# Performance work log

Measured on AMD Instinct MI355X. Metric: run time of the kernel, lower is better.

The kernel has to match this reference:

```python
import jax, jax.numpy as jnp
from jax import lax
import numpy as np

BETA = 1.0


def setup_inputs() -> dict:
    key = jax.random.key(0)
    k1, k2, k3, k4, k5, k6 = jax.random.split(key, 6)
    B, S, D = 16, 2048, 768
    encoder_outputs = jax.random.normal(k1, (B, S, D), dtype=jnp.float32)
    encoder_lens = jax.random.randint(k2, (B,), 1, S + 1, dtype=jnp.int32)
    # AlphaNetwork params: Conv1d(D, D, kernel=3, padding same) + Linear(D, 1)
    conv_w = jax.random.normal(k3, (D, D, 3), dtype=jnp.float32) * (1.0 / np.sqrt(3 * D))
    conv_b = jax.random.normal(k4, (D,), dtype=jnp.float32) * 0.01
    lin_w = jax.random.normal(k5, (1, D), dtype=jnp.float32) * (1.0 / np.sqrt(D))
    lin_b = jax.random.normal(k6, (1,), dtype=jnp.float32) * 0.01
    return {"encoder_outputs": encoder_outputs, "encoder_lens": encoder_lens,
            "conv_w": conv_w, "conv_b": conv_b, "lin_w": lin_w, "lin_b": lin_b}


def _alpha_network(x, conv_w, conv_b, lin_w, lin_b):
    # x: (B, S, D) -> alphas (B, S)
    x_ncw = jnp.transpose(x, (0, 2, 1))  # (B, D, S)
    y = lax.conv_general_dilated(x_ncw, conv_w, window_strides=(1,), padding="SAME",
                                 dimension_numbers=("NCH", "OIH", "NCH"))
    y = y + conv_b[None, :, None]
    y = jnp.transpose(y, (0, 2, 1))  # (B, S, D)
    return jax.nn.sigmoid(jnp.einsum("bsd,od->bso", y, lin_w) + lin_b)[..., 0]


def _cif_single(h, alpha, length, beta=BETA):
    # h: (S, D), alpha: (S,), length: scalar int
    S, D = h.shape

    def step(carry, inputs):
        aacc, hacc = carry
        a_u, h_u, t = inputs
        valid = t < length
        aacc_u = aacc + a_u
        fire = (aacc_u >= beta) & valid
        a1 = 1.0 - aacc               # weight assigned to h_u for the emitted segment
        c = hacc + a1 * h_u           # emitted vector on fire
        a2 = a_u - a1                 # leftover weight carried to next segment
        new_aacc = jnp.where(fire, a2, jnp.where(valid, aacc_u, aacc))
        new_hacc = jnp.where(fire, a2 * h_u, jnp.where(valid, hacc + a_u * h_u, hacc))
        return (new_aacc, new_hacc), (fire, jnp.where(fire, c, jnp.zeros_like(c)))

    init = (jnp.zeros((), h.dtype), jnp.zeros((D,), h.dtype))
    _, (fired, cs) = lax.scan(step, init, (alpha, h, jnp.arange(S)))
    # compact fired vectors to the front; non-fired rows scatter to dropped bucket S
    pos = jnp.cumsum(fired.astype(jnp.int32)) - 1
    idx = jnp.where(fired, pos, S)
    out = jnp.zeros((S + 1, D), h.dtype).at[idx].set(cs)[:S]
    return out, jnp.sum(fired.astype(jnp.int32))


def reference(encoder_outputs, encoder_lens, conv_w, conv_b, lin_w, lin_b):
    alphas = _alpha_network(encoder_outputs, conv_w, conv_b, lin_w, lin_b)  # (B, S)
    output_c, len_tensor = jax.vmap(_cif_single)(encoder_outputs, alphas, encoder_lens)
    # output_c padded to seq_len (static upper bound on number of fires)
    return output_c, len_tensor
```

## Files before the change

### kernel.cpp

```cpp
#include <hip/hip_runtime.h>
#include <math.h>

#define BB 16
#define SS 2048
#define DD 768
#define NROW (BB * SS)
#define NSLICE 16

#define PART_OFF  0
#define W3_OFF    (PART_OFF + NSLICE*2304)
#define BIAS_OFF  (W3_OFF + 2304)
#define E0_OFF    (BIAS_OFF + 64)
#define E1_OFF    (E0_OFF + NROW)
#define E2_OFF    (E1_OFF + NROW)
#define WCUR_OFF  (E2_OFF + NROW)
#define WNEXT_OFF (WCUR_OFF + NROW)
#define FT_OFF    (WNEXT_OFF + NROW)
#define LEN_OFF   (FT_OFF + NROW)

__global__ __launch_bounds__(256) void k1a_fold_part(
    const float* __restrict__ conv_w, const float* __restrict__ lin_w,
    float* __restrict__ ws) {
  int tid = threadIdx.x;
  int slice = blockIdx.x / 9, cb = blockIdx.x % 9;
  int c = cb * 256 + tid;
  int o0 = slice * (DD / NSLICE);
  float acc = 0.f;
#pragma unroll 4
  for (int oo = 0; oo < DD / NSLICE; ++oo) {
    int o = o0 + oo;
    acc = fmaf(lin_w[o], conv_w[(size_t)o * 2304 + c], acc);
  }
  ws[PART_OFF + slice * 2304 + c] = acc;
}

__global__ __launch_bounds__(256) void k1r_fold_reduce(
    const float* __restrict__ conv_b, const float* __restrict__ lin_w,
    const float* __restrict__ lin_b, float* __restrict__ ws) {
  __shared__ float red[256];
  int tid = threadIdx.x;
  if (blockIdx.x < 9) {
    int c = blockIdx.x * 256 + tid;
    float acc = 0.f;
#pragma unroll
    for (int s = 0; s < NSLICE; ++s) acc += ws[PART_OFF + s * 2304 + c];
    int i = c / 3, k = c % 3;
    ws[W3_OFF + k * DD + i] = acc;
  } else {
    float p = 0.f;
    for (int o = tid; o < DD; o += 256) p = fmaf(lin_w[o], conv_b[o], p);
    red[tid] = p;
    __syncthreads();
    for (int off = 128; off > 0; off >>= 1) {
      if (tid < off) red[tid] += red[tid + off];
      __syncthreads();
    }
    if (tid == 0) ws[BIAS_OFF] = red[0] + lin_b[0];
  }
}

__global__ __launch_bounds__(256) void k2a_dots(
    const float* __restrict__ x, const float* __restrict__ ws,
    const int* __restrict__ lens,
    float* __restrict__ e0, float* __restrict__ e1, float* __restrict__ e2) {
  __shared__ float w3[2304];
  int tid = threadIdx.x;
  int wave = tid >> 6, lane = tid & 63;
  int row = blockIdx.x * 4 + wave;
  int b = row >> 11, s = row & (SS - 1);
  bool active = (s <= lens[b]);
  for (int c = tid; c < 2304; c += 256) w3[c] = ws[W3_OFF + c];
  __syncthreads();
  if (!active) return;
  const float4* xr = (const float4*)(x + (size_t)row * DD);
  const float4* w0p = (const float4*)(w3);
  const float4* w1p = (const float4*)(w3 + DD);
  const float4* w2p = (const float4*)(w3 + 2 * DD);
  float a0 = 0.f, a1 = 0.f, a2 = 0.f;
#pragma unroll
  for (int q = 0; q < 3; ++q) {
    int f = lane + q * 64;
    float4 xv = xr[f];
    float4 w0 = w0p[f], w1 = w1p[f], w2 = w2p[f];
    a0 += w0.x * xv.x + w0.y * xv.y + w0.z * xv.z + w0.w * xv.w;
    a1 += w1.x * xv.x + w1.y * xv.y + w1.z * xv.z + w1.w * xv.w;
    a2 += w2.x * xv.x + w2.y * xv.y + w2.z * xv.z + w2.w * xv.w;
  }
#pragma unroll
  for (int m = 1; m < 64; m <<= 1) {
    a0 += __shfl_xor(a0, m);
    a1 += __shfl_xor(a1, m);
    a2 += __shfl_xor(a2, m);
  }
  if (lane == 0) { e0[row] = a0; e1[row] = a1; e2[row] = a2; }
}

__global__ __launch_bounds__(256) void k3_scan(
    const float* __restrict__ ws_ro, const int* __restrict__ lens,
    float* __restrict__ wcur, float* __restrict__ wnext, int* __restrict__ ft,
    int* __restrict__ lenws, float* __restrict__ out_len) {
  __shared__ double wtot[4];
  int b = blockIdx.x, tid = threadIdx.x;
  int wave = tid >> 6, lane = tid & 63;
  const float* e0 = ws_ro + E0_OFF + b * SS;
  const float* e1 = ws_ro + E1_OFF + b * SS;
  const float* e2 = ws_ro + E2_OFF + b * SS;
  float bias = ws_ro[BIAS_OFF];
  int len = lens[b];
  int t0 = tid * 8;
  float a[8];
  double incl[8];
  double run = 0.0;
#pragma unroll
  for (int e = 0; e < 8; ++e) {
    int t = t0 + e;
    float av = 0.f;
    if (t < len) {
      float z = bias + e1[t];
      if (t > 0) z += e0[t - 1];
      z += e2[t + 1];
      av = 1.f / (1.f + expf(-z));
    }
    a[e] = av;
    run += (double)av;
    incl[e] = run;
  }
  double v = run;
#pragma unroll
  for (int m = 1; m < 64; m <<= 1) {
    double o = __shfl_up(v, m);
    if (lane >= m) v += o;
  }
  if (lane == 63) wtot[wave] = v;
  __syncthreads();
  double woff = 0.0;
  for (int w = 0; w < wave; ++w) woff += wtot[w];
  double excl = woff + v - run;
  double Pprev = excl;
  int Fprev = (int)floor(excl);
#pragma unroll
  for (int e = 0; e < 8; ++e) {
    int t = t0 + e;
    double P = excl + incl[e];
    int F = (int)floor(P);
    bool fire = (F > Fprev);
    float wc = fire ? (float)((double)F - Pprev) : a[e];
    float wn = fire ? (float)(P - (double)F) : 0.f;
    wcur[b * SS + t] = wc;
    wnext[b * SS + t] = wn;
    if (fire) ft[b * SS + (F - 1)] = t;
    Pprev = P;
    Fprev = F;
  }
  if (tid == 255) {
    int L = (int)floor(woff + v);
    lenws[b] = L;
    out_len[b] = (float)L;
  }
}

__global__ __launch_bounds__(256) void k4_emit(
    const float* __restrict__ x, const float* __restrict__ wcur,
    const float* __restrict__ wnext, const int* __restrict__ ft,
    const int* __restrict__ lenws, float* __restrict__ out) {
  int tid = threadIdx.x, wave = tid >> 6, lane = tid & 63;
  int row = blockIdx.x * 4 + wave;
  int b = row >> 11, j = row & (SS - 1);
  float4* orow = (float4*)(out + (size_t)row * DD);
  int L = lenws[b];
  if (j >= L) {
    float4 z = {0.f, 0.f, 0.f, 0.f};
    orow[lane] = z;
    orow[lane + 64] = z;
    orow[lane + 128] = z;
    return;
  }
  int start = (j == 0) ? 0 : ft[b * SS + j - 1];
  int end = ft[b * SS + j];
  float4 acc0 = {0, 0, 0, 0}, acc1 = {0, 0, 0, 0}, acc2 = {0, 0, 0, 0};
  for (int t = start; t <= end; ++t) {
    float w = (j > 0 && t == start) ? wnext[b * SS + t] : wcur[b * SS + t];
    const float4* xr = (const float4*)(x + ((size_t)b * SS + t) * DD);
    float4 v0 = xr[lane], v1 = xr[lane + 64], v2 = xr[lane + 128];
    acc0.x = fmaf(w, v0.x, acc0.x); acc0.y = fmaf(w, v0.y, acc0.y);
    acc0.z = fmaf(w, v0.z, acc0.z); acc0.w = fmaf(w, v0.w, acc0.w);
    acc1.x = fmaf(w, v1.x, acc1.x); acc1.y = fmaf(w, v1.y, acc1.y);
    acc1.z = fmaf(w, v1.z, acc1.z); acc1.w = fmaf(w, v1.w, acc1.w);
    acc2.x = fmaf(w, v2.x, acc2.x); acc2.y = fmaf(w, v2.y, acc2.y);
    acc2.z = fmaf(w, v2.z, acc2.z); acc2.w = fmaf(w, v2.w, acc2.w);
  }
  orow[lane] = acc0;
  orow[lane + 64] = acc1;
  orow[lane + 128] = acc2;
}

extern "C" void kernel_launch(void* const* d_in, const int* in_sizes, int n_in,
                              void* d_out, int out_size, void* d_ws, size_t ws_size,
                              hipStream_t stream) {
  const float* x      = (const float*)d_in[0];
  const int*   lens   = (const int*)d_in[1];
  const float* conv_w = (const float*)d_in[2];
  const float* conv_b = (const float*)d_in[3];
  const float* lin_w  = (const float*)d_in[4];
  const float* lin_b  = (const float*)d_in[5];
  float* out = (float*)d_out;
  float* ws = (float*)d_ws;

  float* e0 = ws + E0_OFF;
  float* e1 = ws + E1_OFF;
  float* e2 = ws + E2_OFF;
  float* wc = ws + WCUR_OFF;
  float* wn = ws + WNEXT_OFF;
  int* ft = (int*)(ws + FT_OFF);
  int* lenws = (int*)(ws + LEN_OFF);
  float* out_len = out + (size_t)NROW * DD;

  k1a_fold_part<<<NSLICE * 9, 256, 0, stream>>>(conv_w, lin_w, ws);
  k1r_fold_reduce<<<10, 256, 0, stream>>>(conv_b, lin_w, lin_b, ws);
  k2a_dots<<<NROW / 4, 256, 0, stream>>>(x, ws, lens, e0, e1, e2);
  k3_scan<<<BB, 256, 0, stream>>>(ws, lens, wc, wn, ft, lenws, out_len);
  k4_emit<<<NROW / 4, 256, 0, stream>>>(x, wc, wn, ft, lenws, out);
}
```

Measured before the change: 202.4 us.

## Fuse dot and scan kernels via last-block atomic counter, pack weights, nontemporal stores

Merges the per-row dot-product kernel and the per-batch scan kernel into one launch. Each block bumps a per-batch atomic counter, and the last block to arrive for a batch runs the scan, which removes a kernel launch and its serialization gap. The current and next weights are packed into one float2 array so the emit loop does a single load. The emit kernel now writes its outputs with nontemporal stores and uses native vector FMAs. The cost is that 16 blocks run a serial scan at the tail of a large grid, which could lengthen the critical path.

```diff
diff --git a/kernel.cpp b/kernel.cpp
--- a/kernel.cpp
+++ b/kernel.cpp
@@ -7,21 +7,24 @@
 #define NROW (BB * SS)
 #define NSLICE 16
 
+typedef float nfloat4 __attribute__((ext_vector_type(4)));
+
 #define PART_OFF  0
 #define W3_OFF    (PART_OFF + NSLICE*2304)
 #define BIAS_OFF  (W3_OFF + 2304)
-#define E0_OFF    (BIAS_OFF + 64)
+#define CNT_OFF   (BIAS_OFF + 64)
+#define E0_OFF    (CNT_OFF + 64)
 #define E1_OFF    (E0_OFF + NROW)
 #define E2_OFF    (E1_OFF + NROW)
-#define WCUR_OFF  (E2_OFF + NROW)
-#define WNEXT_OFF (WCUR_OFF + NROW)
-#define FT_OFF    (WNEXT_OFF + NROW)
+#define WPK_OFF   (E2_OFF + NROW)
+#define FT_OFF    (WPK_OFF + 2*NROW)
 #define LEN_OFF   (FT_OFF + NROW)
 
 __global__ __launch_bounds__(256) void k1a_fold_part(
     const float* __restrict__ conv_w, const float* __restrict__ lin_w,
     float* __restrict__ ws) {
   int tid = threadIdx.x;
+  if (blockIdx.x == 0 && tid < BB) ((int*)ws)[CNT_OFF + tid] = 0;
   int slice = blockIdx.x / 9, cb = blockIdx.x % 9;
   int c = cb * 256 + tid;
   int o0 = slice * (DD / NSLICE);
@@ -59,55 +62,69 @@
   }
 }
 
-__global__ __launch_bounds__(256) void k2a_dots(
-    const float* __restrict__ x, const float* __restrict__ ws,
-    const int* __restrict__ lens,
-    float* __restrict__ e0, float* __restrict__ e1, float* __restrict__ e2) {
+__global__ __launch_bounds__(256) void k2_dots_scan(
+    const float* __restrict__ x, const int* __restrict__ lens,
+    float* __restrict__ ws, float* __restrict__ out) {
   __shared__ float w3[2304];
-  int tid = threadIdx.x;
-  int wave = tid >> 6, lane = tid & 63;
-  int row = blockIdx.x * 4 + wave;
-  int b = row >> 11, s = row & (SS - 1);
-  bool active = (s <= lens[b]);
-  for (int c = tid; c < 2304; c += 256) w3[c] = ws[W3_OFF + c];
-  __syncthreads();
-  if (!active) return;
-  const float4* xr = (const float4*)(x + (size_t)row * DD);
-  const float4* w0p = (const float4*)(w3);
-  const float4* w1p = (const float4*)(w3 + DD);
-  const float4* w2p = (const float4*)(w3 + 2 * DD);
-  float a0 = 0.f, a1 = 0.f, a2 = 0.f;
-#pragma unroll
-  for (int q = 0; q < 3; ++q) {
-    int f = lane + q * 64;
-    float4 xv = xr[f];
-    float4 w0 = w0p[f], w1 = w1p[f], w2 = w2p[f];
-    a0 += w0.x * xv.x + w0.y * xv.y + w0.z * xv.z + w0.w * xv.w;
-    a1 += w1.x * xv.x + w1.y * xv.y + w1.z * xv.z + w1.w * xv.w;
-    a2 += w2.x * xv.x + w2.y * xv.y + w2.z * xv.z + w2.w * xv.w;
-  }
-#pragma unroll
-  for (int m = 1; m < 64; m <<= 1) {
-    a0 += __shfl_xor(a0, m);
-    a1 += __shfl_xor(a1, m);
-    a2 += __shfl_xor(a2, m);
-  }
-  if (lane == 0) { e0[row] = a0; e1[row] = a1; e2[row] = a2; }
-}
-
-__global__ __launch_bounds__(256) void k3_scan(
-    const float* __restrict__ ws_ro, const int* __restrict__ lens,
-    float* __restrict__ wcur, float* __restrict__ wnext, int* __restrict__ ft,
-    int* __restrict__ lenws, float* __restrict__ out_len) {
   __shared__ double wtot[4];
-  int b = blockIdx.x, tid = threadIdx.x;
-  int wave = tid >> 6, lane = tid & 63;
-  const float* e0 = ws_ro + E0_OFF + b * SS;
-  const float* e1 = ws_ro + E1_OFF + b * SS;
-  const float* e2 = ws_ro + E2_OFF + b * SS;
-  float bias = ws_ro[BIAS_OFF];
-  int len = lens[b];
-  int t0 = tid * 8;
+  __shared__ int oldc;
+  const int tid = threadIdx.x, wave = tid >> 6, lane = tid & 63;
+  const int blk = blockIdx.x;
+  const int b = blk >> 9;
+  const int len = lens[b];
+  const int baseS = (blk & 511) * 4;
+
+  if (baseS <= len) {
+    for (int c = tid; c < 2304; c += 256) w3[c] = ws[W3_OFF + c];
+    __syncthreads();
+    const int s = baseS + wave;
+    if (s <= len) {
+      const int row = b * SS + s;
+      const float4* xr = (const float4*)(x + (size_t)row * DD);
+      const float4* w0p = (const float4*)(w3);
+      const float4* w1p = (const float4*)(w3 + DD);
+      const float4* w2p = (const float4*)(w3 + 2 * DD);
+      float a0 = 0.f, a1 = 0.f, a2 = 0.f;
+#pragma unroll
+      for (int q = 0; q < 3; ++q) {
+        int f = lane + q * 64;
+        float4 xv = xr[f];
+        float4 w0 = w0p[f], w1 = w1p[f], w2 = w2p[f];
+        a0 += w0.x * xv.x + w0.y * xv.y + w0.z * xv.z + w0.w * xv.w;
+        a1 += w1.x * xv.x + w1.y * xv.y + w1.z * xv.z + w1.w * xv.w;
+        a2 += w2.x * xv.x + w2.y * xv.y + w2.z * xv.z + w2.w * xv.w;
+      }
+#pragma unroll
+      for (int m = 1; m < 64; m <<= 1) {
+        a0 += __shfl_xor(a0, m);
+        a1 += __shfl_xor(a1, m);
+        a2 += __shfl_xor(a2, m);
+      }
+      if (lane == 0) {
+        ws[E0_OFF + row] = a0;
+        ws[E1_OFF + row] = a1;
+        ws[E2_OFF + row] = a2;
+      }
+    }
+  }
+  __syncthreads();
+  if (tid == 0)
+    oldc = __hip_atomic_fetch_add(((int*)ws) + CNT_OFF + b, 1,
+                                  __ATOMIC_RELEASE, __HIP_MEMORY_SCOPE_AGENT);
+  __syncthreads();
+  if (oldc != 511) return;
+  if (tid == 0)
+    (void)__hip_atomic_load(((int*)ws) + CNT_OFF + b,
+                            __ATOMIC_ACQUIRE, __HIP_MEMORY_SCOPE_AGENT);
+  __syncthreads();
+
+  const float* e0 = ws + E0_OFF + b * SS;
+  const float* e1 = ws + E1_OFF + b * SS;
+  const float* e2 = ws + E2_OFF + b * SS;
+  float2* wpk = (float2*)(ws + WPK_OFF) + b * SS;
+  int* ft = ((int*)ws) + FT_OFF + b * SS;
+  const float bias = ws[BIAS_OFF];
+  const int t0 = tid * 8;
   float a[8];
   double incl[8];
   double run = 0.0;
@@ -118,7 +135,7 @@
     if (t < len) {
       float z = bias + e1[t];
       if (t > 0) z += e0[t - 1];
-      z += e2[t + 1];
+      if (t < SS - 1) z += e2[t + 1];
       av = 1.f / (1.f + expf(-z));
     }
     a[e] = av;
@@ -144,54 +161,53 @@
     double P = excl + incl[e];
     int F = (int)floor(P);
     bool fire = (F > Fprev);
-    float wc = fire ? (float)((double)F - Pprev) : a[e];
-    float wn = fire ? (float)(P - (double)F) : 0.f;
-    wcur[b * SS + t] = wc;
-    wnext[b * SS + t] = wn;
-    if (fire) ft[b * SS + (F - 1)] = t;
+    float2 wv;
+    wv.x = fire ? (float)((double)F - Pprev) : a[e];
+    wv.y = fire ? (float)(P - (double)F) : 0.f;
+    wpk[t] = wv;
+    if (fire) ft[F - 1] = t;
     Pprev = P;
     Fprev = F;
   }
   if (tid == 255) {
     int L = (int)floor(woff + v);
-    lenws[b] = L;
-    out_len[b] = (float)L;
+    ((int*)ws)[LEN_OFF + b] = L;
+    out[(size_t)NROW * DD + b] = (float)L;
   }
 }
 
 __global__ __launch_bounds__(256) void k4_emit(
-    const float* __restrict__ x, const float* __restrict__ wcur,
-    const float* __restrict__ wnext, const int* __restrict__ ft,
-    const int* __restrict__ lenws, float* __restrict__ out) {
+    const float* __restrict__ x, const float* __restrict__ ws_ro,
+    float* __restrict__ out) {
   int tid = threadIdx.x, wave = tid >> 6, lane = tid & 63;
   int row = blockIdx.x * 4 + wave;
   int b = row >> 11, j = row & (SS - 1);
-  float4* orow = (float4*)(out + (size_t)row * DD);
-  int L = lenws[b];
+  nfloat4* orow = (nfloat4*)(out + (size_t)row * DD);
+  int L = ((const int*)ws_ro)[LEN_OFF + b];
   if (j >= L) {
-    float4 z = {0.f, 0.f, 0.f, 0.f};
-    orow[lane] = z;
-    orow[lane + 64] = z;
-    orow[lane + 128] = z;
+    nfloat4 z = {0.f, 0.f, 0.f, 0.f};
+    __builtin_nontemporal_store(z, orow + lane);
+    __builtin_nontemporal_store(z, orow + lane + 64);
+    __builtin_nontemporal_store(z, orow + lane + 128);
     return;
   }
-  int start = (j == 0) ? 0 : ft[b * SS + j - 1];
-  int end = ft[b * SS + j];
-  float4 acc0 = {0, 0, 0, 0}, acc1 = {0, 0, 0, 0}, acc2 = {0, 0, 0, 0};
+  const int* ft = ((const int*)ws_ro) + FT_OFF + b * SS;
+  const float2* wpk = (const float2*)(ws_ro + WPK_OFF) + b * SS;
+  int start = (j == 0) ? 0 : ft[j - 1];
+  int end = ft[j];
+  nfloat4 acc0 = {0, 0, 0, 0}, acc1 = {0, 0, 0, 0}, acc2 = {0, 0, 0, 0};
   for (int t = start; t <= end; ++t) {
-    float w = (j > 0 && t == start) ? wnext[b * SS + t] : wcur[b * SS + t];
-    const float4* xr = (const float4*)(x + ((size_t)b * SS + t) * DD);
-    float4 v0 = xr[lane], v1 = xr[lane + 64], v2 = xr[lane + 128];
-    acc0.x = fmaf(w, v0.x, acc0.x); acc0.y = fmaf(w, v0.y, acc0.y);
-    acc0.z = fmaf(w, v0.z, acc0.z); acc0.w = fmaf(w, v0.w, acc0.w);
-    acc1.x = fmaf(w, v1.x, acc1.x); acc1.y = fmaf(w, v1.y, acc1.y);
-    acc1.z = fmaf(w, v1.z, acc1.z); acc1.w = fmaf(w, v1.w, acc1.w);
-    acc2.x = fmaf(w, v2.x, acc2.x); acc2.y = fmaf(w, v2.y, acc2.y);
-    acc2.z = fmaf(w, v2.z, acc2.z); acc2.w = fmaf(w, v2.w, acc2.w);
-  }
-  orow[lane] = acc0;
-  orow[lane + 64] = acc1;
-  orow[lane + 128] = acc2;
+    float2 wv = wpk[t];
+    float w = (j > 0 && t == start) ? wv.y : wv.x;
+    const nfloat4* xr = (const nfloat4*)(x + ((size_t)b * SS + t) * DD);
+    nfloat4 v0 = xr[lane], v1 = xr[lane + 64], v2 = xr[lane + 128];
+    acc0 += w * v0;
+    acc1 += w * v1;
+    acc2 += w * v2;
+  }
+  __builtin_nontemporal_store(acc0, orow + lane);
+  __builtin_nontemporal_store(acc1, orow + lane + 64);
+  __builtin_nontemporal_store(acc2, orow + lane + 128);
 }
 
 extern "C" void kernel_launch(void* const* d_in, const int* in_sizes, int n_in,
@@ -206,18 +222,8 @@
   float* out = (float*)d_out;
   float* ws = (float*)d_ws;
 
-  float* e0 = ws + E0_OFF;
-  float* e1 = ws + E1_OFF;
-  float* e2 = ws + E2_OFF;
-  float* wc = ws + WCUR_OFF;
-  float* wn = ws + WNEXT_OFF;
-  int* ft = (int*)(ws + FT_OFF);
-  int* lenws = (int*)(ws + LEN_OFF);
-  float* out_len = out + (size_t)NROW * DD;
-
   k1a_fold_part<<<NSLICE * 9, 256, 0, stream>>>(conv_w, lin_w, ws);
   k1r_fold_reduce<<<10, 256, 0, stream>>>(conv_b, lin_w, lin_b, ws);
-  k2a_dots<<<NROW / 4, 256, 0, stream>>>(x, ws, lens, e0, e1, e2);
-  k3_scan<<<BB, 256, 0, stream>>>(ws, lens, wc, wn, ft, lenws, out_len);
-  k4_emit<<<NROW / 4, 256, 0, stream>>>(x, wc, wn, ft, lenws, out);
-}
+  k2_dots_scan<<<NROW / 4, 256, 0, stream>>>(x, lens, ws, out);
+  k4_emit<<<NROW / 4, 256, 0, stream>>>(x, ws, out);
+}
```

After: 444.7 us. 2.2x slower.
